# Kernel tuning notes

Hardware: AMD Instinct MI355X
Metric: run time of the kernel (lower is better)

Reference implementation:

```python
import jax, jax.numpy as jnp
import numpy as np

MIN_VAL = 0.0
MAX_VAL = 1.0
NUM_BINS = 512
NUM_NODES = 128
GRAD_SMOOTH = 0.01
BIN_W = (MAX_VAL - MIN_VAL) / NUM_BINS


def _make_kernels():
    sobel = jnp.array([-1.0, 0.0, 1.0], dtype=jnp.float32) / (2.0 * BIN_W)
    r = max(1, int(GRAD_SMOOTH / BIN_W))  # kernel radius in bins
    idx = jnp.arange(2 * r + 1, dtype=jnp.float32) - r
    sigma = GRAD_SMOOTH / BIN_W
    g = jnp.exp(-0.5 * (idx / sigma) ** 2)
    return sobel, g / jnp.sum(g)


def _conv1d_reflect(x, k):
    # x: [N, B], k: [K]; torch Conv1d = cross-correlation with reflect padding
    pad = (k.shape[0] - 1) // 2
    xp = jnp.pad(x, ((0, 0), (pad, pad)), mode='reflect')
    out = jax.lax.conv_general_dilated(
        xp[:, None, :], k[None, None, :], (1,), 'VALID',
        dimension_numbers=('NCH', 'OIH', 'NCH'))
    return out[:, 0, :]


def _compute_cdf_pdf(residuals, weights, src_indices, dst_indices):
    # histogram bin per sample (floor)
    bi = jnp.floor((residuals - MIN_VAL) / BIN_W).astype(jnp.int32)
    valid = (bi >= 0) & (bi < NUM_BINS)
    bi = jnp.clip(bi, 0, NUM_BINS - 1)
    wc = (weights * valid).reshape(-1)  # [N_pairs*K]

    src_comb = (src_indices[:, None] * NUM_BINS + bi).reshape(-1)
    dst_comb = (dst_indices[:, None] * NUM_BINS + bi).reshape(-1)
    nseg = NUM_NODES * NUM_BINS
    hist = (jax.ops.segment_sum(wc, src_comb, num_segments=nseg)
            + jax.ops.segment_sum(wc, dst_comb, num_segments=nseg))
    hist = hist.reshape(NUM_NODES, NUM_BINS)

    wflat = weights.reshape(-1)
    src_exp = jnp.broadcast_to(src_indices[:, None], residuals.shape).reshape(-1)
    dst_exp = jnp.broadcast_to(dst_indices[:, None], residuals.shape).reshape(-1)
    tw = (jax.ops.segment_sum(wflat, src_exp, num_segments=NUM_NODES)
          + jax.ops.segment_sum(wflat, dst_exp, num_segments=NUM_NODES))

    pmf = hist / (tw[:, None] + 1e-10)
    cdf = jnp.cumsum(pmf, axis=1)
    sobel, gauss = _make_kernels()
    pdf = _conv1d_reflect(_conv1d_reflect(cdf, sobel), gauss)
    return cdf, pdf


def _lookup(residuals, weights, cdf, pdf, src_indices, dst_indices):
    # rounded bin for lookup (floor of x + 0.5)
    bi = jnp.floor((residuals - MIN_VAL) / BIN_W + 0.5).astype(jnp.int32)
    valid = (bi >= 0) & (bi < NUM_BINS) & (weights > 0.0)
    bi = jnp.clip(bi, 0, NUM_BINS - 1)
    src_cdf = cdf[src_indices[:, None], bi]
    dst_cdf = cdf[dst_indices[:, None], bi]
    src_grad = pdf[src_indices[:, None], bi] * weights
    dst_grad = pdf[dst_indices[:, None], bi] * weights
    two = jnp.float32(2.0)
    return (jnp.where(valid, src_cdf, two),
            jnp.where(valid, src_grad, 0.0),
            jnp.where(valid, dst_cdf, two),
            jnp.where(valid, dst_grad, 0.0))


def setup_inputs() -> dict:
    key = jax.random.key(0)
    k1, k2, k3, k4 = jax.random.split(key, 4)
    N_pairs, K = 1024, 16384
    return {
        'residuals': jax.random.uniform(k1, (N_pairs, K), dtype=jnp.float32),
        'weights': jax.random.uniform(k2, (N_pairs, K), dtype=jnp.float32),
        'src_indices': jax.random.randint(k3, (N_pairs,), 0, NUM_NODES),
        'dst_indices': jax.random.randint(k4, (N_pairs,), 0, NUM_NODES),
    }


def reference(residuals, weights, src_indices, dst_indices):
    cdf, pdf = _compute_cdf_pdf(residuals, weights, src_indices, dst_indices)
    src_cdf, _, dst_cdf, _ = _lookup(residuals, weights, cdf, pdf,
                                     src_indices, dst_indices)
    return src_cdf, dst_cdf
```

## Files before the change

### kernel.cpp

```cpp
#include <hip/hip_runtime.h>

#define NUM_BINS  512
#define NUM_NODES 128
#define K_ELEMS   16384
#define N_PAIRS   1024
#define NCOPY     32

typedef float f32x4 __attribute__((ext_vector_type(4)));
typedef unsigned int   u32;
typedef unsigned short u16;

__device__ __forceinline__ void gfadd(float* p, float v) { unsafeAtomicAdd(p, v); }

__global__ __launch_bounds__(256) void zero_ws_kernel(float* __restrict__ ws, int n)
{
    int i = blockIdx.x * 256 + threadIdx.x;
    if (i < n) ws[i] = 0.0f;
}

__global__ __launch_bounds__(1024) void hist_kernel(
    const float* __restrict__ residuals, const float* __restrict__ weights,
    const int* __restrict__ src, const int* __restrict__ dst,
    float* __restrict__ hist, float* __restrict__ tw,
    u16* __restrict__ codes)
{
    __shared__ u32 lh[NUM_BINS * NCOPY];
    __shared__ float swsum[16];
    const int row  = blockIdx.x;
    const int t    = threadIdx.x;
    const int copy = t & 31;

    uint4* lh4 = (uint4*)lh;
    #pragma unroll
    for (int k = 0; k < NUM_BINS * NCOPY / 4 / 1024; ++k) {
        uint4 z; z.x = z.y = z.z = z.w = 0u;
        lh4[t + k * 1024] = z;
    }
    __syncthreads();

    const f32x4* r4 = (const f32x4*)(residuals + (size_t)row * K_ELEMS);
    const f32x4* w4 = (const f32x4*)(weights   + (size_t)row * K_ELEMS);
    ushort4*     c4 = (ushort4*)(codes + (size_t)row * K_ELEMS);

    float wsum = 0.0f;
    #pragma unroll
    for (int it = 0; it < K_ELEMS / 4 / 1024; ++it) {
        f32x4 r = __builtin_nontemporal_load(r4 + (t + it * 1024));
        f32x4 w = __builtin_nontemporal_load(w4 + (t + it * 1024));
        wsum += w[0] + w[1] + w[2] + w[3];

        ushort4 cv;
        u16* cp = (u16*)&cv;
        #pragma unroll
        for (int c = 0; c < 4; ++c) {
            int b = (int)floorf(r[c] * 512.0f);
            if ((unsigned)b < 512u)
                atomicAdd(&lh[b * NCOPY + copy], (u32)fmaf(w[c], 65536.0f, 0.5f));
            int lb = (int)floorf(r[c] * 512.0f + 0.5f);
            cp[c] = (u16)((((unsigned)lb < 512u) & (w[c] > 0.0f)) ? lb : 0xFFFF);
        }
        c4[t + it * 1024] = cv;
    }

    #pragma unroll
    for (int off = 32; off > 0; off >>= 1) wsum += __shfl_down(wsum, off, 64);
    const int wave = t >> 6, lane = t & 63;
    if (lane == 0) swsum[wave] = wsum;
    __syncthreads();

    const int s = src[row], d = dst[row];
    if (t == 0) {
        float tot = 0.0f;
        #pragma unroll
        for (int i = 0; i < 16; ++i) tot += swsum[i];
        gfadd(&tw[s], tot);
        gfadd(&tw[d], tot);
    }

    {
        const int bin  = t >> 1;
        const int half = t & 1;
        u32 tot = 0;
        #pragma unroll
        for (int cc = 0; cc < 16; ++cc)
            tot += lh[bin * NCOPY + (((bin + cc) & 15) | (half << 4))];
        tot += (u32)__shfl_xor((int)tot, 1);
        float v = (float)tot * (1.0f / 65536.0f);
        if (half == 0) gfadd(&hist[s * NUM_BINS + bin], v);
        else           gfadd(&hist[d * NUM_BINS + bin], v);
    }
}

__global__ __launch_bounds__(512) void scan_kernel(float* __restrict__ hist,
                                                   const float* __restrict__ tw)
{
    __shared__ float s[NUM_BINS];
    const int node = blockIdx.x;
    const int t    = threadIdx.x;

    const float denom = tw[node] + 1e-10f;
    s[t] = hist[node * NUM_BINS + t] / denom;
    __syncthreads();

    for (int off = 1; off < NUM_BINS; off <<= 1) {
        float add = (t >= off) ? s[t - off] : 0.0f;
        __syncthreads();
        s[t] += add;
        __syncthreads();
    }
    hist[node * NUM_BINS + t] = s[t];
}

__global__ __launch_bounds__(256) void lookup_code_kernel(
    const u16* __restrict__ codes,
    const int* __restrict__ src, const int* __restrict__ dst,
    const float* __restrict__ cdf,
    float* __restrict__ out_src, float* __restrict__ out_dst)
{
    __shared__ float scdf[NUM_BINS];
    __shared__ float dcdf[NUM_BINS];
    const int CHUNK = K_ELEMS / 4;
    const int row   = blockIdx.x >> 2;
    const int chunk = blockIdx.x & 3;
    const int t     = threadIdx.x;

    const int s = src[row], d = dst[row];
    for (int i = t; i < NUM_BINS; i += 256) {
        scdf[i] = cdf[s * NUM_BINS + i];
        dcdf[i] = cdf[d * NUM_BINS + i];
    }
    __syncthreads();

    const size_t base = (size_t)row * K_ELEMS + (size_t)chunk * CHUNK;
    const ushort4* c4 = (const ushort4*)(codes + base);
    f32x4*        os4 = (f32x4*)(out_src + base);
    f32x4*        od4 = (f32x4*)(out_dst + base);

    for (int i = t; i < CHUNK / 4; i += 256) {
        ushort4 c = c4[i];
        f32x4 osv, odv;
        osv[0] = (c.x != 0xFFFF) ? scdf[c.x] : 2.0f;
        odv[0] = (c.x != 0xFFFF) ? dcdf[c.x] : 2.0f;
        osv[1] = (c.y != 0xFFFF) ? scdf[c.y] : 2.0f;
        odv[1] = (c.y != 0xFFFF) ? dcdf[c.y] : 2.0f;
        osv[2] = (c.z != 0xFFFF) ? scdf[c.z] : 2.0f;
        odv[2] = (c.z != 0xFFFF) ? dcdf[c.z] : 2.0f;
        osv[3] = (c.w != 0xFFFF) ? scdf[c.w] : 2.0f;
        odv[3] = (c.w != 0xFFFF) ? dcdf[c.w] : 2.0f;
        __builtin_nontemporal_store(osv, os4 + i);
        __builtin_nontemporal_store(odv, od4 + i);
    }
}

extern "C" void kernel_launch(void* const* d_in, const int* in_sizes, int n_in,
                              void* d_out, int out_size, void* d_ws, size_t ws_size,
                              hipStream_t stream)
{
    const float* residuals = (const float*)d_in[0];
    const float* weights   = (const float*)d_in[1];
    const int*   src       = (const int*)d_in[2];
    const int*   dst       = (const int*)d_in[3];

    float* out_src = (float*)d_out;
    float* out_dst = out_src + (size_t)N_PAIRS * K_ELEMS;

    char* ws = (char*)d_ws;
    float* hist  = (float*)ws;
    float* tw    = (float*)(ws + NUM_NODES * NUM_BINS * 4);
    u16*   codes = (u16*)(ws + (4u << 20));

    const int ws_elems = NUM_NODES * NUM_BINS + NUM_NODES;
    zero_ws_kernel<<<(ws_elems + 255) / 256, 256, 0, stream>>>((float*)d_ws, ws_elems);

    hist_kernel<<<N_PAIRS, 1024, 0, stream>>>(residuals, weights, src, dst,
                                              hist, tw, codes);

    scan_kernel<<<NUM_NODES, NUM_BINS, 0, stream>>>(hist, tw);

    lookup_code_kernel<<<N_PAIRS * 4, 256, 0, stream>>>(codes, src, dst, hist,
                                                        out_src, out_dst);
}
```

Measured before the change: 68.91 us.

## Fuse histogram, scan and lookup into one cooperative kernel with register-held codes

Replaces the four-kernel pipeline with a single cooperative kernel of 256 blocks, each handling 4 rows. Lookup codes stay packed in registers instead of going through a global workspace, and grid-wide syncs separate the zero/histogram, scan and lookup phases. The goal is to remove the 32MB codes write and read-back plus the per-kernel launch gaps. In exchange it runs only one block per CU, processes rows serially inside each block, and adds grid-sync overhead, which may reduce memory-level parallelism. The old path remains as a fallback if the cooperative launch fails.

```diff
diff --git a/kernel.cpp b/kernel.cpp
--- a/kernel.cpp
+++ b/kernel.cpp
@@ -1,16 +1,211 @@
 #include <hip/hip_runtime.h>
+#include <hip/hip_cooperative_groups.h>
+
+namespace cg = cooperative_groups;
 
 #define NUM_BINS  512
 #define NUM_NODES 128
 #define K_ELEMS   16384
 #define N_PAIRS   1024
 #define NCOPY     32
+#define NBLK      256
+#define NTHR      1024
+#define ROWS_PB   4
 
 typedef float f32x4 __attribute__((ext_vector_type(4)));
 typedef unsigned int   u32;
 typedef unsigned short u16;
 
 __device__ __forceinline__ void gfadd(float* p, float v) { unsafeAtomicAdd(p, v); }
+
+
+__device__ __forceinline__ void zero_lds(u32* lh, int t)
+{
+    uint4* lh4 = (uint4*)lh;
+    #pragma unroll
+    for (int k = 0; k < NUM_BINS * NCOPY / 4 / NTHR; ++k) {
+        uint4 z; z.x = z.y = z.z = z.w = 0u;
+        lh4[t + k * NTHR] = z;
+    }
+}
+
+__device__ __forceinline__ float hist_row(
+    const float* __restrict__ residuals, const float* __restrict__ weights,
+    int row, int t, int copy, u32* lh, u32 (&pc)[8])
+{
+    const f32x4* r4 = (const f32x4*)(residuals + (size_t)row * K_ELEMS);
+    const f32x4* w4 = (const f32x4*)(weights   + (size_t)row * K_ELEMS);
+    float wsum = 0.0f;
+    #pragma unroll
+    for (int it = 0; it < K_ELEMS / 4 / NTHR; ++it) {
+        f32x4 r = __builtin_nontemporal_load(r4 + (t + it * NTHR));
+        f32x4 w = __builtin_nontemporal_load(w4 + (t + it * NTHR));
+        wsum += w[0] + w[1] + w[2] + w[3];
+        u32 p0 = 0, p1 = 0;
+        #pragma unroll
+        for (int c = 0; c < 4; ++c) {
+            int b = (int)floorf(r[c] * 512.0f);
+            if ((unsigned)b < 512u)
+                atomicAdd(&lh[b * NCOPY + copy], (u32)fmaf(w[c], 65536.0f, 0.5f));
+            int lb = (int)floorf(r[c] * 512.0f + 0.5f);
+            u32 code = (((unsigned)lb < 512u) & (w[c] > 0.0f)) ? (u32)lb : 0xFFFFu;
+            if (c == 0) p0 |= code;
+            if (c == 1) p0 |= code << 16;
+            if (c == 2) p1 |= code;
+            if (c == 3) p1 |= code << 16;
+        }
+        pc[it * 2] = p0; pc[it * 2 + 1] = p1;
+    }
+    return wsum;
+}
+
+__device__ __forceinline__ void flush_row(const u32* lh, float* __restrict__ hist,
+                                          int s, int d, int t)
+{
+    const int bin  = t >> 1;
+    const int half = t & 1;
+    u32 tot = 0;
+    #pragma unroll
+    for (int cc = 0; cc < 16; ++cc)
+        tot += lh[bin * NCOPY + (((bin + cc) & 15) | (half << 4))];
+    tot += (u32)__shfl_xor((int)tot, 1);
+    float v = (float)tot * (1.0f / 65536.0f);
+    if (half == 0) gfadd(&hist[s * NUM_BINS + bin], v);
+    else           gfadd(&hist[d * NUM_BINS + bin], v);
+}
+
+__device__ __forceinline__ void lookup_row(
+    const u32 (&pc)[8], const float* fl, int row, int t,
+    float* __restrict__ out_src, float* __restrict__ out_dst)
+{
+    f32x4* os = (f32x4*)(out_src + (size_t)row * K_ELEMS);
+    f32x4* od = (f32x4*)(out_dst + (size_t)row * K_ELEMS);
+    #pragma unroll
+    for (int it = 0; it < K_ELEMS / 4 / NTHR; ++it) {
+        u32 p0 = pc[it * 2], p1 = pc[it * 2 + 1];
+        u32 c0 = p0 & 0xFFFFu, c1 = p0 >> 16, c2 = p1 & 0xFFFFu, c3 = p1 >> 16;
+        f32x4 osv, odv;
+        osv[0] = (c0 != 0xFFFFu) ? fl[c0] : 2.0f;
+        odv[0] = (c0 != 0xFFFFu) ? fl[512 + c0] : 2.0f;
+        osv[1] = (c1 != 0xFFFFu) ? fl[c1] : 2.0f;
+        odv[1] = (c1 != 0xFFFFu) ? fl[512 + c1] : 2.0f;
+        osv[2] = (c2 != 0xFFFFu) ? fl[c2] : 2.0f;
+        odv[2] = (c2 != 0xFFFFu) ? fl[512 + c2] : 2.0f;
+        osv[3] = (c3 != 0xFFFFu) ? fl[c3] : 2.0f;
+        odv[3] = (c3 != 0xFFFFu) ? fl[512 + c3] : 2.0f;
+        __builtin_nontemporal_store(osv, os + (t + it * NTHR));
+        __builtin_nontemporal_store(odv, od + (t + it * NTHR));
+    }
+}
+
+__global__ __launch_bounds__(NTHR, 4) void fused_kernel(
+    const float* __restrict__ residuals, const float* __restrict__ weights,
+    const int* __restrict__ src, const int* __restrict__ dst,
+    float* __restrict__ hist, float* __restrict__ tw,
+    float* __restrict__ out_src, float* __restrict__ out_dst)
+{
+    cg::grid_group grid = cg::this_grid();
+    __shared__ u32 lh[NUM_BINS * NCOPY];
+    __shared__ float swsum[16];
+    __shared__ float rowtot[ROWS_PB];
+
+    const int blk  = blockIdx.x;
+    const int t    = threadIdx.x;
+    const int copy = t & 31;
+    const int row0 = blk * ROWS_PB;
+
+    int s0 = src[row0],     d0 = dst[row0];
+    int s1 = src[row0 + 1], d1 = dst[row0 + 1];
+    int s2 = src[row0 + 2], d2 = dst[row0 + 2];
+    int s3 = src[row0 + 3], d3 = dst[row0 + 3];
+
+    u32 pc0[8], pc1[8], pc2[8], pc3[8];
+
+    {
+        int i = blk * NTHR + t;
+        if (i < NUM_NODES * NUM_BINS + NUM_NODES) hist[i] = 0.0f;
+    }
+
+    zero_lds(lh, t);
+    __syncthreads();
+    float ws0 = hist_row(residuals, weights, row0, t, copy, lh, pc0);
+    #pragma unroll
+    for (int off = 32; off > 0; off >>= 1) ws0 += __shfl_down(ws0, off, 64);
+    if ((t & 63) == 0) swsum[t >> 6] = ws0;
+    __syncthreads();
+    if (t == 0) {
+        float a = 0.0f;
+        for (int i = 0; i < 16; ++i) a += swsum[i];
+        rowtot[0] = a;
+    }
+
+    grid.sync();
+
+    flush_row(lh, hist, s0, d0, t);
+
+    #define DO_ROW(Q, PC, SS, DD)                                              \
+    {                                                                          \
+        __syncthreads();                                                       \
+        zero_lds(lh, t);                                                       \
+        __syncthreads();                                                       \
+        float wsq = hist_row(residuals, weights, row0 + Q, t, copy, lh, PC);   \
+        for (int off = 32; off > 0; off >>= 1) wsq += __shfl_down(wsq, off, 64);\
+        if ((t & 63) == 0) swsum[t >> 6] = wsq;                                \
+        __syncthreads();                                                       \
+        if (t == 0) {                                                          \
+            float a = 0.0f;                                                    \
+            for (int i = 0; i < 16; ++i) a += swsum[i];                        \
+            rowtot[Q] = a;                                                     \
+        }                                                                      \
+        flush_row(lh, hist, SS, DD, t);                                        \
+    }
+    DO_ROW(1, pc1, s1, d1)
+    DO_ROW(2, pc2, s2, d2)
+    DO_ROW(3, pc3, s3, d3)
+    #undef DO_ROW
+
+    __syncthreads();
+    if (t == 0) {
+        gfadd(&tw[s0], rowtot[0]); gfadd(&tw[d0], rowtot[0]);
+        gfadd(&tw[s1], rowtot[1]); gfadd(&tw[d1], rowtot[1]);
+        gfadd(&tw[s2], rowtot[2]); gfadd(&tw[d2], rowtot[2]);
+        gfadd(&tw[s3], rowtot[3]); gfadd(&tw[d3], rowtot[3]);
+    }
+
+    grid.sync();
+
+    float* fl = (float*)lh;
+    if (blk < NUM_NODES) {
+        const float denom = tw[blk] + 1e-10f;
+        if (t < NUM_BINS) fl[t] = hist[blk * NUM_BINS + t] / denom;
+        __syncthreads();
+        for (int off = 1; off < NUM_BINS; off <<= 1) {
+            float add = (t < NUM_BINS && t >= off) ? fl[t - off] : 0.0f;
+            __syncthreads();
+            if (t < NUM_BINS) fl[t] += add;
+            __syncthreads();
+        }
+        if (t < NUM_BINS) hist[blk * NUM_BINS + t] = fl[t];
+    }
+
+    grid.sync();
+
+    #define LOOKUP_ROW(Q, PC, SS, DD)                                          \
+    {                                                                          \
+        __syncthreads();                                                       \
+        if (t < NUM_BINS) {                                                    \
+            fl[t]            = hist[SS * NUM_BINS + t];                        \
+            fl[NUM_BINS + t] = hist[DD * NUM_BINS + t];                        \
+        }                                                                      \
+        __syncthreads();                                                       \
+        lookup_row(PC, fl, row0 + Q, t, out_src, out_dst);                     \
+    }
+    LOOKUP_ROW(0, pc0, s0, d0)
+    LOOKUP_ROW(1, pc1, s1, d1)
+    LOOKUP_ROW(2, pc2, s2, d2)
+    LOOKUP_ROW(3, pc3, s3, d3)
+    #undef LOOKUP_ROW
+}
 
 __global__ __launch_bounds__(256) void zero_ws_kernel(float* __restrict__ ws, int n)
 {
@@ -48,7 +243,6 @@
         f32x4 r = __builtin_nontemporal_load(r4 + (t + it * 1024));
         f32x4 w = __builtin_nontemporal_load(w4 + (t + it * 1024));
         wsum += w[0] + w[1] + w[2] + w[3];
-
         ushort4 cv;
         u16* cp = (u16*)&cv;
         #pragma unroll
@@ -164,19 +358,25 @@
     float* out_src = (float*)d_out;
     float* out_dst = out_src + (size_t)N_PAIRS * K_ELEMS;
 
-    char* ws = (char*)d_ws;
-    float* hist  = (float*)ws;
-    float* tw    = (float*)(ws + NUM_NODES * NUM_BINS * 4);
-    u16*   codes = (u16*)(ws + (4u << 20));
-
-    const int ws_elems = NUM_NODES * NUM_BINS + NUM_NODES;
-    zero_ws_kernel<<<(ws_elems + 255) / 256, 256, 0, stream>>>((float*)d_ws, ws_elems);
-
-    hist_kernel<<<N_PAIRS, 1024, 0, stream>>>(residuals, weights, src, dst,
-                                              hist, tw, codes);
-
-    scan_kernel<<<NUM_NODES, NUM_BINS, 0, stream>>>(hist, tw);
-
-    lookup_code_kernel<<<N_PAIRS * 4, 256, 0, stream>>>(codes, src, dst, hist,
-                                                        out_src, out_dst);
-}
+    float* hist  = (float*)d_ws;
+    float* tw    = hist + NUM_NODES * NUM_BINS;
+    u16*   codes = (u16*)((char*)d_ws + (4u << 20));
+
+    void* args[] = {
+        (void*)&residuals, (void*)&weights, (void*)&src, (void*)&dst,
+        (void*)&hist, (void*)&tw, (void*)&out_src, (void*)&out_dst
+    };
+    hipError_t e = hipLaunchCooperativeKernel((const void*)fused_kernel,
+                                              dim3(NBLK), dim3(NTHR), args,
+                                              0, stream);
+    if (e != hipSuccess) {
+        (void)hipGetLastError();
+        const int ws_elems = NUM_NODES * NUM_BINS + NUM_NODES;
+        zero_ws_kernel<<<(ws_elems + 255) / 256, 256, 0, stream>>>((float*)d_ws, ws_elems);
+        hist_kernel<<<N_PAIRS, 1024, 0, stream>>>(residuals, weights, src, dst,
+                                                  hist, tw, codes);
+        scan_kernel<<<NUM_NODES, NUM_BINS, 0, stream>>>(hist, tw);
+        lookup_code_kernel<<<N_PAIRS * 4, 256, 0, stream>>>(codes, src, dst, hist,
+                                                            out_src, out_dst);
+    }
+}
```

New measurement: 153.2 us. 122% more time.
